# Optimization experiments

Hardware: AMD Instinct MI355X
Metric: run time of the kernel (lower is better)

The kernel has to match this reference:

```python
import jax, jax.numpy as jnp
import numpy as np

N, E, F_IN, HID, HEADS, NG, NC = 50000, 800000, 128, 64, 4, 64, 10
NEG_SLOPE = 0.2


def gat_conv(h_in, src, dst, W, att_src, att_dst, bias, heads, out_ch, concat, num_nodes):
    # h_in: [N, Fin]; W: [Fin, heads*out_ch]; att_*: [heads, out_ch]; bias: [heads*out_ch] or [out_ch]
    h = (h_in @ W).reshape(num_nodes, heads, out_ch)            # [N,H,C]
    a_src = jnp.sum(h * att_src, axis=-1)                        # [N,H]
    a_dst = jnp.sum(h * att_dst, axis=-1)                        # [N,H]
    alpha = jax.nn.leaky_relu(a_src[src] + a_dst[dst], NEG_SLOPE)  # [Etot,H]
    # softmax over incoming edges per destination node
    amax = jax.ops.segment_max(alpha, dst, num_segments=num_nodes)
    amax = jnp.where(jnp.isfinite(amax), amax, 0.0)
    ex = jnp.exp(alpha - amax[dst])
    denom = jax.ops.segment_sum(ex, dst, num_segments=num_nodes)
    w = ex / (denom[dst] + 1e-16)                                # [Etot,H]
    msg = h[src] * w[:, :, None]                                 # [Etot,H,C]
    out = jax.ops.segment_sum(msg, dst, num_segments=num_nodes)  # [N,H,C]
    out = out.reshape(num_nodes, heads * out_ch) if concat else out.mean(axis=1)
    return out + bias


def setup_inputs() -> dict:
    key = jax.random.key(0)
    ks = jax.random.split(key, 20)
    s = lambda k, shp, f: (jax.random.normal(k, shp, jnp.float32) * f)
    return {
        "x": jax.random.normal(ks[0], (N, F_IN), jnp.float32),
        "edge_index": jax.random.randint(ks[1], (2, E), 0, N, jnp.int32),
        "batch": jax.random.randint(ks[2], (N,), 0, NG, jnp.int32),
        "W_proj": s(ks[3], (F_IN, HID), 0.05), "b_proj": jnp.zeros((HID,), jnp.float32),
        "W1": s(ks[4], (HID, HEADS * HID), 0.05),
        "att_src1": s(ks[5], (HEADS, HID), 0.1), "att_dst1": s(ks[6], (HEADS, HID), 0.1),
        "b1": jnp.zeros((HEADS * HID,), jnp.float32),
        "W2": s(ks[7], (HEADS * HID, HID), 0.05),
        "att_src2": s(ks[8], (1, HID), 0.1), "att_dst2": s(ks[9], (1, HID), 0.1),
        "b2": jnp.zeros((HID,), jnp.float32),
        "W_fc1": s(ks[10], (HID, HID // 2), 0.05), "b_fc1": jnp.zeros((HID // 2,), jnp.float32),
        "W_fc2": s(ks[11], (HID // 2, NC), 0.05), "b_fc2": jnp.zeros((NC,), jnp.float32),
    }


def reference(x, edge_index, batch, W_proj, b_proj, W1, att_src1, att_dst1, b1,
              W2, att_src2, att_dst2, b2, W_fc1, b_fc1, W_fc2, b_fc2):
    n = x.shape[0]
    loops = jnp.arange(n, dtype=edge_index.dtype)  # PyG GATConv add_self_loops=True
    src = jnp.concatenate([edge_index[0], loops])
    dst = jnp.concatenate([edge_index[1], loops])
    h = jax.nn.relu(x @ W_proj + b_proj)                                  # feature_proj + relu
    h = gat_conv(h, src, dst, W1, att_src1, att_dst1, b1, HEADS, HID, True, n)
    h = jax.nn.leaky_relu(h, NEG_SLOPE)                                    # dropout = identity (eval)
    h = gat_conv(h, src, dst, W2, att_src2, att_dst2, b2, 1, HID, False, n)
    h = jax.nn.leaky_relu(h, NEG_SLOPE)
    cnt = jax.ops.segment_sum(jnp.ones((n,), h.dtype), batch, num_segments=NG)
    gmean = jax.ops.segment_sum(h, batch, num_segments=NG) / jnp.maximum(cnt, 1.0)[:, None]
    gmax = jax.ops.segment_max(h, batch, num_segments=NG)
    gmax = jnp.where(jnp.isfinite(gmax), gmax, 0.0)
    g = gmean + gmax
    g = jax.nn.relu(g @ W_fc1 + b_fc1)
    return jax.nn.log_softmax(g @ W_fc2 + b_fc2, axis=1)
```

## Files before the change

kernel.cpp:

```cpp
#include <hip/hip_runtime.h>
#include <math.h>

#define NN 50000
#define EE 800000
#define ET 850000
#define FIN 128
#define HD 64
#define NH 4
#define NGR 64
#define NCL 10
#define NEG 0.2f
#define NBK 196
#define ECH 831

typedef unsigned short u16;
typedef unsigned char u8;
typedef unsigned int u32;
typedef __attribute__((ext_vector_type(8))) short short8;
typedef __attribute__((ext_vector_type(4))) float f32x4;
typedef __attribute__((ext_vector_type(2))) float f32x2;

__device__ __forceinline__ float lrelu(float x){ return x > 0.f ? x : NEG * x; }

__device__ __forceinline__ float wsum(float v){
#pragma unroll
  for (int o = 32; o > 0; o >>= 1) v += __shfl_xor(v, o, 64);
  return v;
}
__device__ __forceinline__ float wmax(float v){
#pragma unroll
  for (int o = 32; o > 0; o >>= 1) v = fmaxf(v, __shfl_xor(v, o, 64));
  return v;
}
__device__ __forceinline__ int wsumi(int v){
#pragma unroll
  for (int o = 32; o > 0; o >>= 1) v += __shfl_xor(v, o, 64);
  return v;
}
__device__ __forceinline__ int esrc(const int* ei, int e){ return e < EE ? ei[e] : e - EE; }
__device__ __forceinline__ int edst(const int* ei, int e){ return e < EE ? ei[EE + e] : e - EE; }

__device__ __forceinline__ unsigned f2key(float f){
  unsigned u = __float_as_uint(f);
  return (u & 0x80000000u) ? ~u : (u | 0x80000000u);
}
__device__ __forceinline__ float key2f(unsigned k){
  return (k & 0x80000000u) ? __uint_as_float(k & 0x7fffffffu) : __uint_as_float(~k);
}

__device__ __forceinline__ u16 f2b(float f){
  u32 u = __float_as_uint(f);
  u32 r = (u + 0x7FFFu + ((u >> 16) & 1u)) >> 16;
  return (u16)r;
}
__device__ __forceinline__ float b2f(u16 b){ return __uint_as_float(((u32)b) << 16); }
__device__ __forceinline__ u32 pkbf16(float lo, float hi){
  u32 r;
  asm("v_cvt_pk_bf16_f32 %0, %1, %2" : "=v"(r) : "v"(lo), "v"(hi));
  return r;
}
__device__ __forceinline__ u8 f2fp8(float f){
  return (u8)__builtin_amdgcn_cvt_pk_fp8_f32(f, 0.f, 0, false);
}
__device__ __forceinline__ int rl(int v, int idx){ return __builtin_amdgcn_readlane(v, idx); }
__device__ __forceinline__ float rlf(float v, int idx){
  return __uint_as_float((u32)__builtin_amdgcn_readlane((int)__float_as_uint(v), idx));
}

__global__ __launch_bounds__(256) void k_b1hist(const int* __restrict__ ei, int* __restrict__ bcnt,
                                                float* __restrict__ zbase, int zcount){
  __shared__ int lc[NBK];
  int t = threadIdx.x, blk = blockIdx.x;
  if (blk >= ECH){
    for (int i = t; i < zcount; i += 256) zbase[i] = 0.f;
    return;
  }
  for (int i = t; i < NBK; i += 256) lc[i] = 0;
  __syncthreads();
#pragma unroll
  for (int k = 0; k < 4; ++k){
    int e = blk*1024 + k*256 + t;
    if (e < ET) atomicAdd(&lc[edst(ei, e) >> 8], 1);
  }
  __syncthreads();
  for (int i = t; i < NBK; i += 256) bcnt[i*ECH + blk] = lc[i];
}

__global__ __launch_bounds__(256) void k_bscana(const int* __restrict__ bcnt, int* __restrict__ btot){
  int b = blockIdx.x, t = threadIdx.x;
  int s = 0;
  for (int j = t; j < ECH; j += 256) s += bcnt[b*ECH + j];
  s = wsumi(s);
  __shared__ int w4[4];
  if ((t & 63) == 0) w4[t >> 6] = s;
  __syncthreads();
  if (t == 0) btot[b] = w4[0] + w4[1] + w4[2] + w4[3];
}

__global__ __launch_bounds__(256) void k_bscanb(const int* __restrict__ bcnt, const int* __restrict__ btot,
                                                int* __restrict__ boff, int* __restrict__ bb){
  int b = blockIdx.x, t = threadIdx.x;
  int pv = (t < b) ? btot[t] : 0;
  int r = wsumi(pv);
  __shared__ int w4[4];
  if ((t & 63) == 0) w4[t >> 6] = r;
  __syncthreads();
  int base = w4[0] + w4[1] + w4[2] + w4[3];
  if (t == 0) bb[b] = base;
  __shared__ int s[256];
  int carry = 0;
  for (int j0 = 0; j0 < ECH; j0 += 256){
    int j = j0 + t;
    int v = (j < ECH) ? bcnt[b*ECH + j] : 0;
    s[t] = v; __syncthreads();
    for (int d = 1; d < 256; d <<= 1){
      int xv = (t >= d) ? s[t-d] : 0;
      __syncthreads();
      s[t] += xv;
      __syncthreads();
    }
    int excl = s[t] - v;
    if (j < ECH) boff[b*ECH + j] = base + carry + excl;
    int tot = s[255];
    __syncthreads();
    carry += tot;
  }
}

__global__ __launch_bounds__(256) void k_b1scat(const int* __restrict__ ei, const int* __restrict__ boff,
                                                u32* __restrict__ packed){
  __shared__ int lpos[NBK];
  int t = threadIdx.x, blk = blockIdx.x;
  for (int i = t; i < NBK; i += 256) lpos[i] = boff[i*ECH + blk];
  __syncthreads();
#pragma unroll
  for (int k = 0; k < 4; ++k){
    int e = blk*1024 + k*256 + t;
    if (e < ET){
      int d = edst(ei, e);
      int s = esrc(ei, e);
      int slot = atomicAdd(&lpos[d >> 8], 1);
      packed[slot] = ((u32)(d & 255) << 16) | (u32)s;
    }
  }
}

__global__ __launch_bounds__(256) void k_phf2(
            const u32* __restrict__ packed, const int* __restrict__ btot, const int* __restrict__ bb,
            int* __restrict__ off, u16* __restrict__ csrc,
            const float* __restrict__ x, const float* __restrict__ Wp, const float* __restrict__ bp,
            const float* __restrict__ W1, const float* __restrict__ as1, const float* __restrict__ ad1,
            u8* __restrict__ h1f8, float* __restrict__ a_s, float* __restrict__ a_d, int gb){
  __shared__ u16 As[64*(FIN+8)];
  __shared__ u16 h0s[64*(HD+8)];
  __shared__ int hc[256];
  __shared__ int sc[256];
  __shared__ int pp[256];
  int t = threadIdx.x;
  int bid = blockIdx.x;
  if (bid >= gb){
    int b = bid - gb;
    int e0 = bb[b];
    int cntb = btot[b];
    hc[t] = 0;
    __syncthreads();
    for (int i = t; i < cntb; i += 256){
      u32 p = packed[e0 + i];
      atomicAdd(&hc[p >> 16], 1);
    }
    __syncthreads();
    int v = hc[t];
    sc[t] = v; __syncthreads();
    for (int d = 1; d < 256; d <<= 1){
      int xv = (t >= d) ? sc[t-d] : 0;
      __syncthreads();
      sc[t] += xv;
      __syncthreads();
    }
    int excl = sc[t] - v;
    int node = b*256 + t;
    if (node < NN) off[node] = e0 + excl;
    if (b == 0 && t == 0) off[NN] = ET;
    pp[t] = excl;
    __syncthreads();
    for (int i = t; i < cntb; i += 256){
      u32 p = packed[e0 + i];
      int slot = atomicAdd(&pp[p >> 16], 1);
      csrc[(size_t)e0 + slot] = (u16)(p & 0xFFFFu);
    }
    return;
  }
  constexpr int LDK1 = FIN + 8;
  constexpr int LDH  = HD + 8;
  int w = t >> 6, l = t & 63;
  int l16 = l & 15, kg = l >> 4;

  short8 bfp[4];
#pragma unroll
  for (int kt = 0; kt < 4; ++kt){
    short8 v;
#pragma unroll
    for (int j = 0; j < 8; ++j) v[j] = (short)f2b(Wp[(size_t)(kt*32 + kg*8 + j)*HD + w*16 + l16]);
    bfp[kt] = v;
  }
  short8 bf1[2*4];
#pragma unroll
  for (int kt = 0; kt < 2; ++kt)
#pragma unroll
    for (int nt = 0; nt < 4; ++nt){
      short8 v;
#pragma unroll
      for (int j = 0; j < 8; ++j) v[j] = (short)f2b(W1[(size_t)(kt*32 + kg*8 + j)*256 + w*64 + nt*16 + l16]);
      bf1[kt*4 + nt] = v;
    }
  float bv = bp[w*16 + l16];
  float asv[4], adv[4];
#pragma unroll
  for (int nt = 0; nt < 4; ++nt){
    asv[nt] = as1[w*64 + nt*16 + l16];
    adv[nt] = ad1[w*64 + nt*16 + l16];
  }

  for (int ch = 0; ch < 2; ++ch){
    int nb = (bid*2 + ch)*64;
    if (nb >= NN) break;
    __syncthreads();
    for (int u = t; u < 64*16; u += 256){
      int r = u >> 4, c = u & 15;
      int n = nb + r;
      uint4 v = make_uint4(0u,0u,0u,0u);
      if (n < NN){
        float4 f0 = *(const float4*)&x[(size_t)n*FIN + c*8];
        float4 f1 = *(const float4*)&x[(size_t)n*FIN + c*8 + 4];
        v = make_uint4(pkbf16(f0.x,f0.y), pkbf16(f0.z,f0.w), pkbf16(f1.x,f1.y), pkbf16(f1.z,f1.w));
      }
      *(uint4*)&As[r*LDK1 + c*8] = v;
    }
    __syncthreads();
#pragma unroll
    for (int rt = 0; rt < 4; ++rt){
      short8 afp[4];
#pragma unroll
      for (int kt = 0; kt < 4; ++kt)
        afp[kt] = *(const short8*)&As[(rt*16 + l16)*LDK1 + kt*32 + kg*8];
      f32x4 acc = (f32x4){0.f,0.f,0.f,0.f};
#pragma unroll
      for (int kt = 0; kt < 4; ++kt)
        acc = __builtin_amdgcn_mfma_f32_16x16x32_bf16(afp[kt], bfp[kt], acc, 0, 0, 0);
#pragma unroll
      for (int r4 = 0; r4 < 4; ++r4)
        h0s[(rt*16 + kg*4 + r4)*LDH + w*16 + l16] = f2b(fmaxf(acc[r4] + bv, 0.f));
    }
    __syncthreads();
#pragma unroll
    for (int rt = 0; rt < 4; ++rt){
      short8 af[2];
#pragma unroll
      for (int kt = 0; kt < 2; ++kt)
        af[kt] = *(const short8*)&h0s[(rt*16 + l16)*LDH + kt*32 + kg*8];
      f32x4 acc[4];
#pragma unroll
      for (int nt = 0; nt < 4; ++nt){
        acc[nt] = (f32x4){0.f,0.f,0.f,0.f};
#pragma unroll
        for (int kt = 0; kt < 2; ++kt)
          acc[nt] = __builtin_amdgcn_mfma_f32_16x16x32_bf16(af[kt], bf1[kt*4 + nt], acc[nt], 0, 0, 0);
      }
      int rbase = nb + rt*16 + kg*4;
#pragma unroll
      for (int nt = 0; nt < 4; ++nt)
#pragma unroll
        for (int r4 = 0; r4 < 4; ++r4){
          int n = rbase + r4;
          if (n < NN) h1f8[(size_t)n*256 + w*64 + nt*16 + l16] = f2fp8(acc[nt][r4]);
        }
#pragma unroll
      for (int r4 = 0; r4 < 4; ++r4){
        float ps = 0.f, pd = 0.f;
#pragma unroll
        for (int nt = 0; nt < 4; ++nt){
          ps = fmaf(acc[nt][r4], asv[nt], ps);
          pd = fmaf(acc[nt][r4], adv[nt], pd);
        }
#pragma unroll
        for (int o = 1; o < 16; o <<= 1){
          ps += __shfl_xor(ps, o, 64);
          pd += __shfl_xor(pd, o, 64);
        }
        int n = rbase + r4;
        if (l16 == 0 && n < NN){ a_s[n*NH + w] = ps; a_d[n*NH + w] = pd; }
      }
    }
  }
}

template<int K, int NOUT, int CPW>
__device__ __forceinline__ void gemm_body2(int bid, u16* As, float* sred,
            const u16* __restrict__ A, const float* __restrict__ Bf,
            const float* __restrict__ att_s, const float* __restrict__ att_d,
            u16* __restrict__ C, float* __restrict__ a_s, float* __restrict__ a_d){
  constexpr int KT = K/32;
  constexpr int LDK = K + 8;
  int t = threadIdx.x, w = t >> 6, l = t & 63;
  int c0 = w*CPW;
  int l16 = l & 15, kg = l >> 4;

  short8 bf[KT];
#pragma unroll
  for (int kt = 0; kt < KT; ++kt){
    int kbase = kt*32 + kg*8;
    int col = c0 + l16;
    short8 v;
#pragma unroll
    for (int j = 0; j < 8; ++j) v[j] = (short)f2b(Bf[(size_t)(kbase + j)*NOUT + col]);
    bf[kt] = v;
  }
  float asv = att_s[c0 + l16], adv = att_d[c0 + l16];

  for (int ch = 0; ch < 2; ++ch){
    int nb = (bid*2 + ch)*64;
    if (nb >= NN) break;
    __syncthreads();
    constexpr int UPR = K/8;
    for (int u = t; u < 64*UPR; u += 256){
      int r = u / UPR, c = u % UPR;
      int n = nb + r;
      uint4 v = make_uint4(0u,0u,0u,0u);
      if (n < NN) v = *(const uint4*)&A[(size_t)n*K + c*8];
      *(uint4*)&As[r*LDK + c*8] = v;
    }
    __syncthreads();
#pragma unroll
    for (int rt = 0; rt < 4; ++rt){
      short8 af[KT];
#pragma unroll
      for (int kt = 0; kt < KT; ++kt)
        af[kt] = *(const short8*)&As[(rt*16 + l16)*LDK + kt*32 + kg*8];
      f32x4 acc = (f32x4){0.f,0.f,0.f,0.f};
#pragma unroll
      for (int kt = 0; kt < KT; ++kt)
        acc = __builtin_amdgcn_mfma_f32_16x16x32_bf16(af[kt], bf[kt], acc, 0, 0, 0);
      int rbase = nb + rt*16 + kg*4;
#pragma unroll
      for (int r4 = 0; r4 < 4; ++r4){
        int n = rbase + r4;
        if (n < NN) C[(size_t)n*NOUT + c0 + l16] = f2b(acc[r4]);
      }
#pragma unroll
      for (int r4 = 0; r4 < 4; ++r4){
        float ps = acc[r4]*asv;
        float pd = acc[r4]*adv;
#pragma unroll
        for (int o = 1; o < 16; o <<= 1){
          ps += __shfl_xor(ps, o, 64);
          pd += __shfl_xor(pd, o, 64);
        }
        if (l16 == 0){
          int row = rt*16 + kg*4 + r4;
          sred[(w*64 + row)*2]     = ps;
          sred[(w*64 + row)*2 + 1] = pd;
        }
      }
    }
    __syncthreads();
    if (t < 64){
      int n = nb + t;
      if (n < NN){
        float s = sred[t*2] + sred[(64+t)*2] + sred[(128+t)*2] + sred[(192+t)*2];
        float d = sred[t*2+1] + sred[(64+t)*2+1] + sred[(128+t)*2+1] + sred[(192+t)*2+1];
        a_s[n] = s; a_d[n] = d;
      }
    }
  }
}

__global__ __launch_bounds__(256) void k_feat2(const u16* __restrict__ h1outb, const float* __restrict__ W2,
            const float* __restrict__ as2, const float* __restrict__ ad2,
            u16* __restrict__ h2b, float* __restrict__ a_s, float* __restrict__ a_d){
  __shared__ u16 As[64*(256+8)];
  __shared__ float sred[4*64*2];
  gemm_body2<256, 64, 16>(blockIdx.x, As, sred, h1outb, W2, as2, ad2, h2b, a_s, a_d);
}

__global__ __launch_bounds__(256) void k_gat1(const u8* __restrict__ h1f8, const float* __restrict__ a_s,
                       const float* __restrict__ a_d, const int* __restrict__ off,
                       const u16* __restrict__ csrc, const float* __restrict__ b1,
                       u16* __restrict__ h1outb){
  __shared__ float lw[4][4][68];
  int wv = threadIdx.x >> 6, l = threadIdx.x & 63;
  int n = blockIdx.x*4 + wv;
  if (n >= NN) return;
  int e0 = off[n], e1 = off[n+1], deg = e1 - e0;
  int j16 = l & 15, h = l >> 4;
  float adst = a_d[n*NH + h];
  float acc0 = 0.f, acc1 = 0.f, acc2 = 0.f, acc3 = 0.f;
  const u8* base = h1f8 + 4*l;

#define GAT1_FMA8(wrd, wq) { \
  f32x2 lo_ = __builtin_amdgcn_cvt_pk_f32_fp8((int)(wrd), false); \
  f32x2 hi_ = __builtin_amdgcn_cvt_pk_f32_fp8((int)(wrd), true); \
  acc0 = fmaf(lo_.x, wq, acc0); acc1 = fmaf(lo_.y, wq, acc1); \
  acc2 = fmaf(hi_.x, wq, acc2); acc3 = fmaf(hi_.y, wq, acc3); }

  if (deg <= 64){
    int sreg[4]; float wreg[4];
#pragma unroll
    for (int c = 0; c < 4; ++c){
      int idx = c*16 + j16;
      int s = (idx < deg) ? (int)csrc[e0 + idx] : 0;
      sreg[c] = s;
      wreg[c] = (idx < deg) ? lrelu(a_s[s*NH + h] + adst) : -3.0e38f;
    }
    float m = fmaxf(fmaxf(wreg[0], wreg[1]), fmaxf(wreg[2], wreg[3]));
#pragma unroll
    for (int o2 = 1; o2 < 16; o2 <<= 1) m = fmaxf(m, __shfl_xor(m, o2, 64));
    float se = 0.f;
#pragma unroll
    for (int c = 0; c < 4; ++c){
      int idx = c*16 + j16;
      float wc = (idx < deg) ? __expf(wreg[c] - m) : 0.f;
      wreg[c] = wc; se += wc;
    }
#pragma unroll
    for (int o2 = 1; o2 < 16; o2 <<= 1) se += __shfl_xor(se, o2, 64);
    float inv = 1.f / (se + 1e-16f);
#pragma unroll
    for (int c = 0; c < 4; ++c) lw[wv][h][c*16 + j16] = wreg[c] * inv;

#pragma unroll
    for (int c = 0; c < 4; ++c){
      int cbase = c*16;
      if (cbase < deg){
        int cnt = deg - cbase; if (cnt > 16) cnt = 16;
        int j2 = 0;
        for (; j2 + 8 <= cnt; j2 += 8){
          float4 wqa = *(const float4*)&lw[wv][h][cbase + j2];
          float4 wqb = *(const float4*)&lw[wv][h][cbase + j2 + 4];
          int s0 = rl(sreg[c], j2),   s1 = rl(sreg[c], j2+1);
          int s2 = rl(sreg[c], j2+2), s3 = rl(sreg[c], j2+3);
          int s4 = rl(sreg[c], j2+4), s5 = rl(sreg[c], j2+5);
          int s6 = rl(sreg[c], j2+6), s7 = rl(sreg[c], j2+7);
          u32 w0 = *(const u32*)(base + (size_t)(u32)s0*256);
          u32 w1 = *(const u32*)(base + (size_t)(u32)s1*256);
          u32 w2 = *(const u32*)(base + (size_t)(u32)s2*256);
          u32 w3 = *(const u32*)(base + (size_t)(u32)s3*256);
          u32 w4 = *(const u32*)(base + (size_t)(u32)s4*256);
          u32 w5 = *(const u32*)(base + (size_t)(u32)s5*256);
          u32 w6 = *(const u32*)(base + (size_t)(u32)s6*256);
          u32 w7 = *(const u32*)(base + (size_t)(u32)s7*256);
          GAT1_FMA8(w0, wqa.x) GAT1_FMA8(w1, wqa.y) GAT1_FMA8(w2, wqa.z) GAT1_FMA8(w3, wqa.w)
          GAT1_FMA8(w4, wqb.x) GAT1_FMA8(w5, wqb.y) GAT1_FMA8(w6, wqb.z) GAT1_FMA8(w7, wqb.w)
        }
        for (; j2 + 4 <= cnt; j2 += 4){
          float4 wq = *(const float4*)&lw[wv][h][cbase + j2];
          int s0 = rl(sreg[c], j2),   s1 = rl(sreg[c], j2+1);
          int s2 = rl(sreg[c], j2+2), s3 = rl(sreg[c], j2+3);
          u32 w0 = *(const u32*)(base + (size_t)(u32)s0*256);
          u32 w1 = *(const u32*)(base + (size_t)(u32)s1*256);
          u32 w2 = *(const u32*)(base + (size_t)(u32)s2*256);
          u32 w3 = *(const u32*)(base + (size_t)(u32)s3*256);
          GAT1_FMA8(w0, wq.x) GAT1_FMA8(w1, wq.y) GAT1_FMA8(w2, wq.z) GAT1_FMA8(w3, wq.w)
        }
        for (; j2 < cnt; ++j2){
          float wqs = lw[wv][h][cbase + j2];
          int s = rl(sreg[c], j2);
          u32 wd = *(const u32*)(base + (size_t)(u32)s*256);
          GAT1_FMA8(wd, wqs)
        }
      }
    }
  } else {
    float m = -3.0e38f;
    for (int i = e0 + j16; i < e1; i += 16){
      int s = csrc[i];
      m = fmaxf(m, lrelu(a_s[s*NH + h] + adst));
    }
#pragma unroll
    for (int o2 = 1; o2 < 16; o2 <<= 1) m = fmaxf(m, __shfl_xor(m, o2, 64));
    float se = 0.f;
    for (int i = e0 + j16; i < e1; i += 16){
      int s = csrc[i];
      se += __expf(lrelu(a_s[s*NH + h] + adst) - m);
    }
#pragma unroll
    for (int o2 = 1; o2 < 16; o2 <<= 1) se += __shfl_xor(se, o2, 64);
    float inv = 1.f / (se + 1e-16f);
    for (int i = e0; i < e1; ++i){
      int s = csrc[i];
      float wq = __expf(lrelu(a_s[s*NH + h] + adst) - m) * inv;
      u32 wd = *(const u32*)(base + (size_t)(u32)s*256);
      GAT1_FMA8(wd, wq)
    }
  }
  float4 bv = *(const float4*)&b1[4*l];
  u32 lo = pkbf16(lrelu(acc0 + bv.x), lrelu(acc1 + bv.y));
  u32 hi = pkbf16(lrelu(acc2 + bv.z), lrelu(acc3 + bv.w));
  *(uint2*)&h1outb[(size_t)n*256 + 4*l] = make_uint2(lo, hi);
}

__global__ __launch_bounds__(256) void k_gat2(const u16* __restrict__ h2b, const float* __restrict__ a_s,
                       const float* __restrict__ a_d, const int* __restrict__ off,
                       const u16* __restrict__ csrc, const float* __restrict__ b2v,
                       u16* __restrict__ h2outb){
  int wv = threadIdx.x >> 6, l = threadIdx.x & 63;
  int n = blockIdx.x*4 + wv;
  if (n >= NN) return;
  int e0 = off[n], e1 = off[n+1], deg = e1 - e0;
  float adst = a_d[n];
  if (deg <= 64){
    int sA = 0; float alA = -3.0e38f;
    if (l < deg){
      sA = (int)csrc[e0 + l];
      alA = lrelu(a_s[sA] + adst);
    }
    float m = wmax(alA);
    float wA = (l < deg) ? __expf(alA - m) : 0.f;
    float se = wsum(wA);
    wA *= 1.f / (se + 1e-16f);
    float acc = 0.f;
    int idx = 0;
    for (; idx + 8 <= deg; idx += 8){
      int s0 = rl(sA, idx),   s1 = rl(sA, idx+1);
      int s2 = rl(sA, idx+2), s3 = rl(sA, idx+3);
      int s4 = rl(sA, idx+4), s5 = rl(sA, idx+5);
      int s6 = rl(sA, idx+6), s7 = rl(sA, idx+7);
      float w0 = rlf(wA, idx),   w1 = rlf(wA, idx+1);
      float w2 = rlf(wA, idx+2), w3 = rlf(wA, idx+3);
      float w4 = rlf(wA, idx+4), w5 = rlf(wA, idx+5);
      float w6 = rlf(wA, idx+6), w7 = rlf(wA, idx+7);
      float v0 = b2f(h2b[(size_t)(u32)s0*HD + l]);
      float v1 = b2f(h2b[(size_t)(u32)s1*HD + l]);
      float v2 = b2f(h2b[(size_t)(u32)s2*HD + l]);
      float v3 = b2f(h2b[(size_t)(u32)s3*HD + l]);
      float v4 = b2f(h2b[(size_t)(u32)s4*HD + l]);
      float v5 = b2f(h2b[(size_t)(u32)s5*HD + l]);
      float v6 = b2f(h2b[(size_t)(u32)s6*HD + l]);
      float v7 = b2f(h2b[(size_t)(u32)s7*HD + l]);
      acc = fmaf(v0, w0, acc); acc = fmaf(v1, w1, acc);
      acc = fmaf(v2, w2, acc); acc = fmaf(v3, w3, acc);
      acc = fmaf(v4, w4, acc); acc = fmaf(v5, w5, acc);
      acc = fmaf(v6, w6, acc); acc = fmaf(v7, w7, acc);
    }
    for (; idx < deg; ++idx){
      int s = rl(sA, idx);
      float w = rlf(wA, idx);
      acc = fmaf(b2f(h2b[(size_t)(u32)s*HD + l]), w, acc);
    }
    h2outb[(size_t)n*HD + l] = f2b(lrelu(acc + b2v[l]));
  } else {
    float m = -3.0e38f;
    for (int i = e0 + l; i < e1; i += 64){
      int s = csrc[i];
      m = fmaxf(m, lrelu(a_s[s] + adst));
    }
    m = wmax(m);
    float se = 0.f;
    for (int i = e0 + l; i < e1; i += 64){
      int s = csrc[i];
      se += __expf(lrelu(a_s[s] + adst) - m);
    }
    se = wsum(se);
    float inv = 1.f / (se + 1e-16f);
    float acc = 0.f;
    for (int i = e0; i < e1; ++i){
      int s = csrc[i];
      acc += b2f(h2b[(size_t)s*HD + l]) * __expf(lrelu(a_s[s] + adst) - m);
    }
    h2outb[(size_t)n*HD + l] = f2b(lrelu(acc*inv + b2v[l]));
  }
}


__global__ void k_pool(const u16* __restrict__ h2outb, const int* __restrict__ batch,
                       float* __restrict__ gsum, unsigned* __restrict__ gmaxk, int* __restrict__ gcnt){
  __shared__ float ssum[NGR*HD];
  __shared__ unsigned smax[NGR*HD];
  __shared__ int scnt[NGR];
  int t = threadIdx.x;
  for (int i = t; i < NGR*HD; i += 256){ ssum[i] = 0.f; smax[i] = 0u; }
  if (t < NGR) scnt[t] = 0;
  __syncthreads();
  int wv = t >> 6, lane = t & 63;
  for (int n = blockIdx.x*4 + wv; n < NN; n += gridDim.x*4){
    int g = batch[n];
    float v = b2f(h2outb[(size_t)n*HD + lane]);
    atomicAdd(&ssum[g*HD + lane], v);
    atomicMax(&smax[g*HD + lane], f2key(v));
    if (lane == 0) atomicAdd(&scnt[g], 1);
  }
  __syncthreads();
  for (int i = t; i < NGR*HD; i += 256){
    atomicAdd(&gsum[i], ssum[i]);
    atomicMax(&gmaxk[i], smax[i]);
  }
  if (t < NGR) atomicAdd(&gcnt[t], scnt[t]);
}


__global__ void k_final(const float* __restrict__ gsum, const unsigned* __restrict__ gmaxk,
                        const int* __restrict__ gcnt,
                        const float* __restrict__ Wf1, const float* __restrict__ bf1,
                        const float* __restrict__ Wf2, const float* __restrict__ bf2,
                        float* __restrict__ out){
  int g = blockIdx.x, t = threadIdx.x;
  __shared__ float gv[HD];
  __shared__ float f1[32];
  __shared__ float lg[NCL];
  int c = gcnt[g];
  float dn = fmaxf((float)c, 1.f);
  float mean = gsum[g*HD + t] / dn;
  float mx = (c > 0) ? key2f(gmaxk[g*HD + t]) : 0.f;
  gv[t] = mean + mx;
  __syncthreads();
  if (t < 32){
    float a = bf1[t];
#pragma unroll
    for (int k = 0; k < HD; ++k) a += gv[k] * Wf1[k*32 + t];
    f1[t] = a > 0.f ? a : 0.f;
  }
  __syncthreads();
  if (t < NCL){
    float a = bf2[t];
#pragma unroll
    for (int k = 0; k < 32; ++k) a += f1[k] * Wf2[k*NCL + t];
    lg[t] = a;
  }
  __syncthreads();
  if (t < NCL){
    float m = lg[0];
#pragma unroll
    for (int i = 1; i < NCL; ++i) m = fmaxf(m, lg[i]);
    float s = 0.f;
#pragma unroll
    for (int i = 0; i < NCL; ++i) s += expf(lg[i] - m);
    out[g*NCL + t] = lg[t] - m - logf(s);
  }
}

extern "C" void kernel_launch(void* const* d_in, const int* in_sizes, int n_in,
                              void* d_out, int out_size, void* d_ws, size_t ws_size,
                              hipStream_t stream) {
  const float* x   = (const float*)d_in[0];
  const int*   ei  = (const int*)d_in[1];
  const int*   bat = (const int*)d_in[2];
  const float* Wp  = (const float*)d_in[3];
  const float* bp  = (const float*)d_in[4];
  const float* W1  = (const float*)d_in[5];
  const float* as1 = (const float*)d_in[6];
  const float* ad1 = (const float*)d_in[7];
  const float* b1  = (const float*)d_in[8];
  const float* W2  = (const float*)d_in[9];
  const float* as2 = (const float*)d_in[10];
  const float* ad2 = (const float*)d_in[11];
  const float* b2  = (const float*)d_in[12];
  const float* Wf1 = (const float*)d_in[13];
  const float* bf1 = (const float*)d_in[14];
  const float* Wf2 = (const float*)d_in[15];
  const float* bf2 = (const float*)d_in[16];
  float* out = (float*)d_out;

  char* base = (char*)d_ws;
  size_t o = 0;
  auto alloc = [&](size_t elems) -> char* {
    char* p = base + o*4;
    o += (elems + 63) & ~(size_t)63;
    return p;
  };
  u8*    h1f8   = (u8*)alloc(3200000);
  u16*   h1outb = (u16*)alloc(6400000);
  u16*   h2b    = (u16*)alloc(1600000);
  u16*   h2outb = (u16*)alloc(1600000);
  float* a_s1   = (float*)alloc(200000);
  float* a_d1   = (float*)alloc(200000);
  float* a_s2   = (float*)alloc(50000);
  float* a_d2   = (float*)alloc(50000);
  int*   off    = (int*)alloc(50001);
  int*   bcnt   = (int*)alloc(NBK*ECH);
  int*   boff   = (int*)alloc(NBK*ECH);
  int*   btot   = (int*)alloc(256);
  int*   bb     = (int*)alloc(256);
  u32*   packed = (u32*)alloc(850000);
  u16*   csrc   = (u16*)alloc(425000);
  char*  zstart = base + o*4;
  float* gsum   = (float*)alloc(NGR*HD);
  unsigned* gmaxk = (unsigned*)alloc(NGR*HD);
  int*   gcnt   = (int*)alloc(NGR);
  int    zcount = (int)(((base + o*4) - zstart) / 4);

  const int GB  = (NN + 127) / 128;
  const int WB  = (NN + 3) / 4;

  k_b1hist<<<ECH + 1, 256, 0, stream>>>(ei, bcnt, (float*)zstart, zcount);
  k_bscana<<<NBK, 256, 0, stream>>>(bcnt, btot);
  k_bscanb<<<NBK, 256, 0, stream>>>(bcnt, btot, boff, bb);
  k_b1scat<<<ECH, 256, 0, stream>>>(ei, boff, packed);

  k_phf2<<<GB + NBK, 256, 0, stream>>>(packed, btot, bb, off, csrc,
                                       x, Wp, bp, W1, as1, ad1, h1f8, a_s1, a_d1, GB);

  k_gat1<<<WB, 256, 0, stream>>>(h1f8, a_s1, a_d1, off, csrc, b1, h1outb);

  k_feat2<<<GB, 256, 0, stream>>>(h1outb, W2, as2, ad2, h2b, a_s2, a_d2);
  k_gat2<<<WB, 256, 0, stream>>>(h2b, a_s2, a_d2, off, csrc, b2, h2outb);

  k_pool<<<256, 256, 0, stream>>>(h2outb, bat, gsum, gmaxk, gcnt);

  k_final<<<NGR, 64, 0, stream>>>(gsum, gmaxk, gcnt, Wf1, bf1, Wf2, bf2, out);
}
```

Baseline: 170.5 us.

## Fuse GAT layer-1 aggregation with layer-2 projection GEMM via shared memory

Merges the layer-1 attention aggregation kernel and the layer-2 feature GEMM into one kernel. Each block aggregates 64 destination nodes (16 per wave) into a bf16 tile in LDS, then runs the MFMA projection and attention-score reduction on that tile. This removes the 25.6 MB h1out round trip through global memory and one kernel launch. In exchange the grid shrinks to about 782 blocks with serial per-wave node loops, and the large LDS tile may lower occupancy, which could hurt latency hiding in the gather-heavy aggregation phase.

```diff
diff --git a/kernel.cpp b/kernel.cpp
--- a/kernel.cpp
+++ b/kernel.cpp
@@ -294,107 +294,21 @@
   }
 }
 
-template<int K, int NOUT, int CPW>
-__device__ __forceinline__ void gemm_body2(int bid, u16* As, float* sred,
-            const u16* __restrict__ A, const float* __restrict__ Bf,
-            const float* __restrict__ att_s, const float* __restrict__ att_d,
-            u16* __restrict__ C, float* __restrict__ a_s, float* __restrict__ a_d){
-  constexpr int KT = K/32;
-  constexpr int LDK = K + 8;
-  int t = threadIdx.x, w = t >> 6, l = t & 63;
-  int c0 = w*CPW;
-  int l16 = l & 15, kg = l >> 4;
-
-  short8 bf[KT];
-#pragma unroll
-  for (int kt = 0; kt < KT; ++kt){
-    int kbase = kt*32 + kg*8;
-    int col = c0 + l16;
-    short8 v;
-#pragma unroll
-    for (int j = 0; j < 8; ++j) v[j] = (short)f2b(Bf[(size_t)(kbase + j)*NOUT + col]);
-    bf[kt] = v;
-  }
-  float asv = att_s[c0 + l16], adv = att_d[c0 + l16];
-
-  for (int ch = 0; ch < 2; ++ch){
-    int nb = (bid*2 + ch)*64;
-    if (nb >= NN) break;
-    __syncthreads();
-    constexpr int UPR = K/8;
-    for (int u = t; u < 64*UPR; u += 256){
-      int r = u / UPR, c = u % UPR;
-      int n = nb + r;
-      uint4 v = make_uint4(0u,0u,0u,0u);
-      if (n < NN) v = *(const uint4*)&A[(size_t)n*K + c*8];
-      *(uint4*)&As[r*LDK + c*8] = v;
-    }
-    __syncthreads();
-#pragma unroll
-    for (int rt = 0; rt < 4; ++rt){
-      short8 af[KT];
-#pragma unroll
-      for (int kt = 0; kt < KT; ++kt)
-        af[kt] = *(const short8*)&As[(rt*16 + l16)*LDK + kt*32 + kg*8];
-      f32x4 acc = (f32x4){0.f,0.f,0.f,0.f};
-#pragma unroll
-      for (int kt = 0; kt < KT; ++kt)
-        acc = __builtin_amdgcn_mfma_f32_16x16x32_bf16(af[kt], bf[kt], acc, 0, 0, 0);
-      int rbase = nb + rt*16 + kg*4;
-#pragma unroll
-      for (int r4 = 0; r4 < 4; ++r4){
-        int n = rbase + r4;
-        if (n < NN) C[(size_t)n*NOUT + c0 + l16] = f2b(acc[r4]);
-      }
-#pragma unroll
-      for (int r4 = 0; r4 < 4; ++r4){
-        float ps = acc[r4]*asv;
-        float pd = acc[r4]*adv;
-#pragma unroll
-        for (int o = 1; o < 16; o <<= 1){
-          ps += __shfl_xor(ps, o, 64);
-          pd += __shfl_xor(pd, o, 64);
-        }
-        if (l16 == 0){
-          int row = rt*16 + kg*4 + r4;
-          sred[(w*64 + row)*2]     = ps;
-          sred[(w*64 + row)*2 + 1] = pd;
-        }
-      }
-    }
-    __syncthreads();
-    if (t < 64){
-      int n = nb + t;
-      if (n < NN){
-        float s = sred[t*2] + sred[(64+t)*2] + sred[(128+t)*2] + sred[(192+t)*2];
-        float d = sred[t*2+1] + sred[(64+t)*2+1] + sred[(128+t)*2+1] + sred[(192+t)*2+1];
-        a_s[n] = s; a_d[n] = d;
-      }
-    }
-  }
-}
-
-__global__ __launch_bounds__(256) void k_feat2(const u16* __restrict__ h1outb, const float* __restrict__ W2,
-            const float* __restrict__ as2, const float* __restrict__ ad2,
-            u16* __restrict__ h2b, float* __restrict__ a_s, float* __restrict__ a_d){
-  __shared__ u16 As[64*(256+8)];
-  __shared__ float sred[4*64*2];
-  gemm_body2<256, 64, 16>(blockIdx.x, As, sred, h1outb, W2, as2, ad2, h2b, a_s, a_d);
-}
-
-__global__ __launch_bounds__(256) void k_gat1(const u8* __restrict__ h1f8, const float* __restrict__ a_s,
+#define LDH1 264
+__global__ __launch_bounds__(256) void k_g1f2(const u8* __restrict__ h1f8, const float* __restrict__ a_s,
                        const float* __restrict__ a_d, const int* __restrict__ off,
                        const u16* __restrict__ csrc, const float* __restrict__ b1,
-                       u16* __restrict__ h1outb){
+                       const float* __restrict__ W2, const float* __restrict__ as2,
+                       const float* __restrict__ ad2,
+                       u16* __restrict__ h2b, float* __restrict__ a_s2o, float* __restrict__ a_d2o){
+  __shared__ u16 h1s[64*LDH1];
   __shared__ float lw[4][4][68];
-  int wv = threadIdx.x >> 6, l = threadIdx.x & 63;
-  int n = blockIdx.x*4 + wv;
-  if (n >= NN) return;
-  int e0 = off[n], e1 = off[n+1], deg = e1 - e0;
+  __shared__ float sred[4*64*2];
+  int t = threadIdx.x, wv = t >> 6, l = t & 63;
   int j16 = l & 15, h = l >> 4;
-  float adst = a_d[n*NH + h];
-  float acc0 = 0.f, acc1 = 0.f, acc2 = 0.f, acc3 = 0.f;
+  int nb = blockIdx.x * 64;
   const u8* base = h1f8 + 4*l;
+  float4 bv = *(const float4*)&b1[4*l];
 
 #define GAT1_FMA8(wrd, wq) { \
   f32x2 lo_ = __builtin_amdgcn_cvt_pk_f32_fp8((int)(wrd), false); \
@@ -402,100 +316,160 @@
   acc0 = fmaf(lo_.x, wq, acc0); acc1 = fmaf(lo_.y, wq, acc1); \
   acc2 = fmaf(hi_.x, wq, acc2); acc3 = fmaf(hi_.y, wq, acc3); }
 
-  if (deg <= 64){
-    int sreg[4]; float wreg[4];
-#pragma unroll
-    for (int c = 0; c < 4; ++c){
-      int idx = c*16 + j16;
-      int s = (idx < deg) ? (int)csrc[e0 + idx] : 0;
-      sreg[c] = s;
-      wreg[c] = (idx < deg) ? lrelu(a_s[s*NH + h] + adst) : -3.0e38f;
-    }
-    float m = fmaxf(fmaxf(wreg[0], wreg[1]), fmaxf(wreg[2], wreg[3]));
-#pragma unroll
-    for (int o2 = 1; o2 < 16; o2 <<= 1) m = fmaxf(m, __shfl_xor(m, o2, 64));
-    float se = 0.f;
-#pragma unroll
-    for (int c = 0; c < 4; ++c){
-      int idx = c*16 + j16;
-      float wc = (idx < deg) ? __expf(wreg[c] - m) : 0.f;
-      wreg[c] = wc; se += wc;
-    }
-#pragma unroll
-    for (int o2 = 1; o2 < 16; o2 <<= 1) se += __shfl_xor(se, o2, 64);
-    float inv = 1.f / (se + 1e-16f);
-#pragma unroll
-    for (int c = 0; c < 4; ++c) lw[wv][h][c*16 + j16] = wreg[c] * inv;
-
-#pragma unroll
-    for (int c = 0; c < 4; ++c){
-      int cbase = c*16;
-      if (cbase < deg){
-        int cnt = deg - cbase; if (cnt > 16) cnt = 16;
-        int j2 = 0;
-        for (; j2 + 8 <= cnt; j2 += 8){
-          float4 wqa = *(const float4*)&lw[wv][h][cbase + j2];
-          float4 wqb = *(const float4*)&lw[wv][h][cbase + j2 + 4];
-          int s0 = rl(sreg[c], j2),   s1 = rl(sreg[c], j2+1);
-          int s2 = rl(sreg[c], j2+2), s3 = rl(sreg[c], j2+3);
-          int s4 = rl(sreg[c], j2+4), s5 = rl(sreg[c], j2+5);
-          int s6 = rl(sreg[c], j2+6), s7 = rl(sreg[c], j2+7);
-          u32 w0 = *(const u32*)(base + (size_t)(u32)s0*256);
-          u32 w1 = *(const u32*)(base + (size_t)(u32)s1*256);
-          u32 w2 = *(const u32*)(base + (size_t)(u32)s2*256);
-          u32 w3 = *(const u32*)(base + (size_t)(u32)s3*256);
-          u32 w4 = *(const u32*)(base + (size_t)(u32)s4*256);
-          u32 w5 = *(const u32*)(base + (size_t)(u32)s5*256);
-          u32 w6 = *(const u32*)(base + (size_t)(u32)s6*256);
-          u32 w7 = *(const u32*)(base + (size_t)(u32)s7*256);
-          GAT1_FMA8(w0, wqa.x) GAT1_FMA8(w1, wqa.y) GAT1_FMA8(w2, wqa.z) GAT1_FMA8(w3, wqa.w)
-          GAT1_FMA8(w4, wqb.x) GAT1_FMA8(w5, wqb.y) GAT1_FMA8(w6, wqb.z) GAT1_FMA8(w7, wqb.w)
+  for (int i = 0; i < 16; ++i){
+    int n = nb + wv*16 + i;
+    if (n >= NN) break;
+    int e0 = off[n], e1 = off[n+1], deg = e1 - e0;
+    float adst = a_d[n*NH + h];
+    float acc0 = 0.f, acc1 = 0.f, acc2 = 0.f, acc3 = 0.f;
+    if (deg <= 64){
+      int sreg[4]; float wreg[4];
+#pragma unroll
+      for (int c = 0; c < 4; ++c){
+        int idx = c*16 + j16;
+        int s = (idx < deg) ? (int)csrc[e0 + idx] : 0;
+        sreg[c] = s;
+        wreg[c] = (idx < deg) ? lrelu(a_s[s*NH + h] + adst) : -3.0e38f;
+      }
+      float m = fmaxf(fmaxf(wreg[0], wreg[1]), fmaxf(wreg[2], wreg[3]));
+#pragma unroll
+      for (int o2 = 1; o2 < 16; o2 <<= 1) m = fmaxf(m, __shfl_xor(m, o2, 64));
+      float se = 0.f;
+#pragma unroll
+      for (int c = 0; c < 4; ++c){
+        int idx = c*16 + j16;
+        float wc = (idx < deg) ? __expf(wreg[c] - m) : 0.f;
+        wreg[c] = wc; se += wc;
+      }
+#pragma unroll
+      for (int o2 = 1; o2 < 16; o2 <<= 1) se += __shfl_xor(se, o2, 64);
+      float inv = 1.f / (se + 1e-16f);
+#pragma unroll
+      for (int c = 0; c < 4; ++c) lw[wv][h][c*16 + j16] = wreg[c] * inv;
+
+#pragma unroll
+      for (int c = 0; c < 4; ++c){
+        int cbase = c*16;
+        if (cbase < deg){
+          int cnt = deg - cbase; if (cnt > 16) cnt = 16;
+          int j2 = 0;
+          for (; j2 + 8 <= cnt; j2 += 8){
+            float4 wqa = *(const float4*)&lw[wv][h][cbase + j2];
+            float4 wqb = *(const float4*)&lw[wv][h][cbase + j2 + 4];
+            int s0 = rl(sreg[c], j2),   s1 = rl(sreg[c], j2+1);
+            int s2 = rl(sreg[c], j2+2), s3 = rl(sreg[c], j2+3);
+            int s4 = rl(sreg[c], j2+4), s5 = rl(sreg[c], j2+5);
+            int s6 = rl(sreg[c], j2+6), s7 = rl(sreg[c], j2+7);
+            u32 w0 = *(const u32*)(base + (size_t)(u32)s0*256);
+            u32 w1 = *(const u32*)(base + (size_t)(u32)s1*256);
+            u32 w2 = *(const u32*)(base + (size_t)(u32)s2*256);
+            u32 w3 = *(const u32*)(base + (size_t)(u32)s3*256);
+            u32 w4 = *(const u32*)(base + (size_t)(u32)s4*256);
+            u32 w5 = *(const u32*)(base + (size_t)(u32)s5*256);
+            u32 w6 = *(const u32*)(base + (size_t)(u32)s6*256);
+            u32 w7 = *(const u32*)(base + (size_t)(u32)s7*256);
+            GAT1_FMA8(w0, wqa.x) GAT1_FMA8(w1, wqa.y) GAT1_FMA8(w2, wqa.z) GAT1_FMA8(w3, wqa.w)
+            GAT1_FMA8(w4, wqb.x) GAT1_FMA8(w5, wqb.y) GAT1_FMA8(w6, wqb.z) GAT1_FMA8(w7, wqb.w)
+          }
+          for (; j2 + 4 <= cnt; j2 += 4){
+            float4 wq = *(const float4*)&lw[wv][h][cbase + j2];
+            int s0 = rl(sreg[c], j2),   s1 = rl(sreg[c], j2+1);
+            int s2 = rl(sreg[c], j2+2), s3 = rl(sreg[c], j2+3);
+            u32 w0 = *(const u32*)(base + (size_t)(u32)s0*256);
+            u32 w1 = *(const u32*)(base + (size_t)(u32)s1*256);
+            u32 w2 = *(const u32*)(base + (size_t)(u32)s2*256);
+            u32 w3 = *(const u32*)(base + (size_t)(u32)s3*256);
+            GAT1_FMA8(w0, wq.x) GAT1_FMA8(w1, wq.y) GAT1_FMA8(w2, wq.z) GAT1_FMA8(w3, wq.w)
+          }
+          for (; j2 < cnt; ++j2){
+            float wqs = lw[wv][h][cbase + j2];
+            int s = rl(sreg[c], j2);
+            u32 wd = *(const u32*)(base + (size_t)(u32)s*256);
+            GAT1_FMA8(wd, wqs)
+          }
         }
-        for (; j2 + 4 <= cnt; j2 += 4){
-          float4 wq = *(const float4*)&lw[wv][h][cbase + j2];
-          int s0 = rl(sreg[c], j2),   s1 = rl(sreg[c], j2+1);
-          int s2 = rl(sreg[c], j2+2), s3 = rl(sreg[c], j2+3);
-          u32 w0 = *(const u32*)(base + (size_t)(u32)s0*256);
-          u32 w1 = *(const u32*)(base + (size_t)(u32)s1*256);
-          u32 w2 = *(const u32*)(base + (size_t)(u32)s2*256);
-          u32 w3 = *(const u32*)(base + (size_t)(u32)s3*256);
-          GAT1_FMA8(w0, wq.x) GAT1_FMA8(w1, wq.y) GAT1_FMA8(w2, wq.z) GAT1_FMA8(w3, wq.w)
-        }
-        for (; j2 < cnt; ++j2){
-          float wqs = lw[wv][h][cbase + j2];
-          int s = rl(sreg[c], j2);
-          u32 wd = *(const u32*)(base + (size_t)(u32)s*256);
-          GAT1_FMA8(wd, wqs)
-        }
-      }
-    }
-  } else {
-    float m = -3.0e38f;
-    for (int i = e0 + j16; i < e1; i += 16){
-      int s = csrc[i];
-      m = fmaxf(m, lrelu(a_s[s*NH + h] + adst));
-    }
-#pragma unroll
-    for (int o2 = 1; o2 < 16; o2 <<= 1) m = fmaxf(m, __shfl_xor(m, o2, 64));
-    float se = 0.f;
-    for (int i = e0 + j16; i < e1; i += 16){
-      int s = csrc[i];
-      se += __expf(lrelu(a_s[s*NH + h] + adst) - m);
-    }
-#pragma unroll
-    for (int o2 = 1; o2 < 16; o2 <<= 1) se += __shfl_xor(se, o2, 64);
-    float inv = 1.f / (se + 1e-16f);
-    for (int i = e0; i < e1; ++i){
-      int s = csrc[i];
-      float wq = __expf(lrelu(a_s[s*NH + h] + adst) - m) * inv;
-      u32 wd = *(const u32*)(base + (size_t)(u32)s*256);
-      GAT1_FMA8(wd, wq)
-    }
-  }
-  float4 bv = *(const float4*)&b1[4*l];
-  u32 lo = pkbf16(lrelu(acc0 + bv.x), lrelu(acc1 + bv.y));
-  u32 hi = pkbf16(lrelu(acc2 + bv.z), lrelu(acc3 + bv.w));
-  *(uint2*)&h1outb[(size_t)n*256 + 4*l] = make_uint2(lo, hi);
+      }
+    } else {
+      float m = -3.0e38f;
+      for (int i2 = e0 + j16; i2 < e1; i2 += 16){
+        int s = csrc[i2];
+        m = fmaxf(m, lrelu(a_s[s*NH + h] + adst));
+      }
+#pragma unroll
+      for (int o2 = 1; o2 < 16; o2 <<= 1) m = fmaxf(m, __shfl_xor(m, o2, 64));
+      float se = 0.f;
+      for (int i2 = e0 + j16; i2 < e1; i2 += 16){
+        int s = csrc[i2];
+        se += __expf(lrelu(a_s[s*NH + h] + adst) - m);
+      }
+#pragma unroll
+      for (int o2 = 1; o2 < 16; o2 <<= 1) se += __shfl_xor(se, o2, 64);
+      float inv = 1.f / (se + 1e-16f);
+      for (int i2 = e0; i2 < e1; ++i2){
+        int s = csrc[i2];
+        float wq = __expf(lrelu(a_s[s*NH + h] + adst) - m) * inv;
+        u32 wd = *(const u32*)(base + (size_t)(u32)s*256);
+        GAT1_FMA8(wd, wq)
+      }
+    }
+    u32 lo = pkbf16(lrelu(acc0 + bv.x), lrelu(acc1 + bv.y));
+    u32 hi = pkbf16(lrelu(acc2 + bv.z), lrelu(acc3 + bv.w));
+    int r = wv*16 + i;
+    *(uint2*)&h1s[r*LDH1 + 4*l] = make_uint2(lo, hi);
+  }
+  __syncthreads();
+
+  int l16 = l & 15, kg = l >> 4;
+  short8 bf[8];
+#pragma unroll
+  for (int kt = 0; kt < 8; ++kt){
+    short8 v;
+#pragma unroll
+    for (int j = 0; j < 8; ++j) v[j] = (short)f2b(W2[(size_t)(kt*32 + kg*8 + j)*HD + wv*16 + l16]);
+    bf[kt] = v;
+  }
+  float asv = as2[wv*16 + l16], adv = ad2[wv*16 + l16];
+#pragma unroll
+  for (int rt = 0; rt < 4; ++rt){
+    short8 af[8];
+#pragma unroll
+    for (int kt = 0; kt < 8; ++kt)
+      af[kt] = *(const short8*)&h1s[(rt*16 + l16)*LDH1 + kt*32 + kg*8];
+    f32x4 acc = (f32x4){0.f,0.f,0.f,0.f};
+#pragma unroll
+    for (int kt = 0; kt < 8; ++kt)
+      acc = __builtin_amdgcn_mfma_f32_16x16x32_bf16(af[kt], bf[kt], acc, 0, 0, 0);
+    int rbase = nb + rt*16 + kg*4;
+#pragma unroll
+    for (int r4 = 0; r4 < 4; ++r4){
+      int n = rbase + r4;
+      if (n < NN) h2b[(size_t)n*HD + wv*16 + l16] = f2b(acc[r4]);
+    }
+#pragma unroll
+    for (int r4 = 0; r4 < 4; ++r4){
+      float ps = acc[r4]*asv;
+      float pd = acc[r4]*adv;
+#pragma unroll
+      for (int o = 1; o < 16; o <<= 1){
+        ps += __shfl_xor(ps, o, 64);
+        pd += __shfl_xor(pd, o, 64);
+      }
+      if (l16 == 0){
+        int row = rt*16 + kg*4 + r4;
+        sred[(wv*64 + row)*2]     = ps;
+        sred[(wv*64 + row)*2 + 1] = pd;
+      }
+    }
+  }
+  __syncthreads();
+  if (t < 64){
+    int n = nb + t;
+    if (n < NN){
+      float s = sred[t*2] + sred[(64+t)*2] + sred[(128+t)*2] + sred[(192+t)*2];
+      float d = sred[t*2+1] + sred[(64+t)*2+1] + sred[(128+t)*2+1] + sred[(192+t)*2+1];
+      a_s2o[n] = s; a_d2o[n] = d;
+    }
+  }
 }
 
 __global__ __launch_bounds__(256) void k_gat2(const u16* __restrict__ h2b, const float* __restrict__ a_s,
@@ -667,7 +641,6 @@
     return p;
   };
   u8*    h1f8   = (u8*)alloc(3200000);
-  u16*   h1outb = (u16*)alloc(6400000);
   u16*   h2b    = (u16*)alloc(1600000);
   u16*   h2outb = (u16*)alloc(1600000);
   float* a_s1   = (float*)alloc(200000);
@@ -688,6 +661,7 @@
   int    zcount = (int)(((base + o*4) - zstart) / 4);
 
   const int GB  = (NN + 127) / 128;
+  const int NB2 = (NN + 63) / 64;
   const int WB  = (NN + 3) / 4;
 
   k_b1hist<<<ECH + 1, 256, 0, stream>>>(ei, bcnt, (float*)zstart, zcount);
@@ -698,9 +672,8 @@
   k_phf2<<<GB + NBK, 256, 0, stream>>>(packed, btot, bb, off, csrc,
                                        x, Wp, bp, W1, as1, ad1, h1f8, a_s1, a_d1, GB);
 
-  k_gat1<<<WB, 256, 0, stream>>>(h1f8, a_s1, a_d1, off, csrc, b1, h1outb);
-
-  k_feat2<<<GB, 256, 0, stream>>>(h1outb, W2, as2, ad2, h2b, a_s2, a_d2);
+  k_g1f2<<<NB2, 256, 0, stream>>>(h1f8, a_s1, a_d1, off, csrc, b1, W2, as2, ad2, h2b, a_s2, a_d2);
+
   k_gat2<<<WB, 256, 0, stream>>>(h2b, a_s2, a_d2, off, csrc, b2, h2outb);
 
   k_pool<<<256, 256, 0, stream>>>(h2outb, bat, gsum, gmaxk, gcnt);
```

New measurement: 185.4 us. +8.7%, slower.
